# Performance work log

Hardware: AMD Instinct MI355X
Metric: run time of the kernel (lower is better)

Reference implementation:

```python
import jax, jax.numpy as jnp
import numpy as np

N = 50000      # nodes
E = 1600000    # edges (before self loops)
IN = 128
OUT = 128
H = 4
HD = OUT // H  # head dim = 32


def setup_inputs() -> dict:
    key = jax.random.key(0)
    k1, k2, k3, k4, k5 = jax.random.split(key, 5)
    x = jax.random.normal(k1, (N, IN), dtype=jnp.float32)
    edge_index = jax.random.randint(k2, (2, E), 0, N, dtype=jnp.int64)
    # xavier-uniform-ish scales
    W = jax.random.normal(k3, (OUT, IN), dtype=jnp.float32) * (1.0 / np.sqrt(IN))
    att_src = jax.random.normal(k4, (1, H, HD), dtype=jnp.float32) * 0.1
    att_dst = jax.random.normal(k5, (1, H, HD), dtype=jnp.float32) * 0.1
    return {"x": x, "edge_index": edge_index, "W": W, "att_src": att_src, "att_dst": att_dst}


def reference(x, edge_index, W, att_src, att_dst):
    n = x.shape[0]
    # add self loops (tg.utils.add_self_loops appends [i, i] edges)
    loops = jnp.arange(n, dtype=edge_index.dtype)
    ei = jnp.concatenate([edge_index, jnp.stack([loops, loops])], axis=1)
    src, dst = ei[0], ei[1]

    # linear projection, split into heads: [n, H, HD]
    h = (x @ W.T).reshape(n, H, HD)

    # per-node attention logits per head: [n, H]
    a_src = jnp.sum(h * att_src, axis=-1)
    a_dst = jnp.sum(h * att_dst, axis=-1)

    # per-edge attention score: gather + leaky_relu
    alpha = a_src[src] + a_dst[dst]                      # [Etot, H]
    alpha = jax.nn.leaky_relu(alpha, negative_slope=0.2)

    # segment softmax grouped by destination node (numerically stable)
    m = jax.ops.segment_max(alpha, dst, num_segments=n)  # [n, H]
    e = jnp.exp(alpha - m[dst])
    s = jax.ops.segment_sum(e, dst, num_segments=n)      # [n, H]
    e = e / s[dst]                                       # [Etot, H]

    # weighted scatter-add aggregation; f_additive adds 1 to the weights
    msg = h[src] * (e[:, :, None] + 1.0)                 # [Etot, H, HD]
    out = jax.ops.segment_sum(msg, dst, num_segments=n)  # [n, H, HD]
    return out.reshape(n, -1)
```

## Files before the change

### kernel.cpp

```cpp
#include <hip/hip_runtime.h>

#define N_NODES 50000
#define E_EDGES 1600000
#define ETOT    (E_EDGES + N_NODES)
#define DIN  128
#define DOUT 128
#define NH   4
#define HD   32

typedef unsigned short ushort_t;
typedef unsigned int uint_t;
typedef __attribute__((ext_vector_type(8))) short bfrag;
typedef __attribute__((ext_vector_type(4))) float ffrag;

__device__ __forceinline__ ushort_t f2bf(float f) {
  uint_t u = __float_as_uint(f);
  u += 0x7fffu + ((u >> 16) & 1u);
  return (ushort_t)(u >> 16);
}
__device__ __forceinline__ float bf_lo(uint_t u) {
  return __uint_as_float(u << 16);
}
__device__ __forceinline__ float bf_hi(uint_t u) {
  return __uint_as_float(u & 0xffff0000u);
}

#define BSZ   64
#define NBUCK ((N_NODES + BSZ - 1) / BSZ)
#define NBP   1024
#define CAP   2560
#define EPB_A 8192
#define NBLK_A ((ETOT + EPB_A - 1) / EPB_A)
#define NCHUNK 13


__global__ __launch_bounds__(256, 4) void fused_binA_gemm_kernel(
    const int* __restrict__ ei, uint_t* __restrict__ ebuf,
    int* __restrict__ cntm, int* __restrict__ offm,
    const float* __restrict__ x, const float* __restrict__ W,
    const float* __restrict__ att_src, const float* __restrict__ att_dst,
    ushort_t* __restrict__ hb, float* __restrict__ a_src,
    float* __restrict__ a_dst) {
  __shared__ uint_t lds[EPB_A + NBP + 8];
  const int tid = threadIdx.x;

  if (blockIdx.x < NBLK_A) {
    uint_t* stage = lds;
    int* hist = (int*)(lds + EPB_A);
    int* wsum = hist + NBP;
    const int cb = blockIdx.x;
    const int e0 = cb * EPB_A;
    const int n = min(EPB_A, ETOT - e0);
    for (int i = tid; i < NBP; i += 256) hist[i] = 0;
    __syncthreads();
    for (int i = tid; i < n; i += 256) {
      int e = e0 + i;
      int si, di;
      if (e < E_EDGES) { si = ei[e]; di = ei[E_EDGES + e]; }
      else             { si = e - E_EDGES; di = si; }
      stage[i] = ((uint_t)di << 16) | (uint_t)si;
      atomicAdd(&hist[di >> 6], 1);
    }
    __syncthreads();
    const int ln = tid & 63, wv = tid >> 6;
    int c0 = hist[4 * tid], c1 = hist[4 * tid + 1];
    int c2 = hist[4 * tid + 2], c3 = hist[4 * tid + 3];
    int p1 = c0, p2 = c0 + c1, p3 = c0 + c1 + c2;
    int tot = p3 + c3;
    int xx = tot;
#pragma unroll
    for (int off = 1; off < 64; off <<= 1) {
      int y = __shfl_up(xx, off, 64);
      if (ln >= off) xx += y;
    }
    if (ln == 63) wsum[wv] = xx;
    __syncthreads();
    if (tid < 4) {
      int w = wsum[tid];
#pragma unroll
      for (int off = 1; off < 4; off <<= 1) {
        int y = __shfl_up(w, off, 64);
        if (tid >= off) w += y;
      }
      wsum[tid] = w;
    }
    __syncthreads();
    const int wo = (wv == 0) ? 0 : wsum[wv - 1];
    const int base = wo + xx - tot;
#pragma unroll
    for (int k = 0; k < 4; k++) {
      int idx = 4 * tid + k;
      int c = k == 0 ? c0 : k == 1 ? c1 : k == 2 ? c2 : c3;
      int o = base + (k == 0 ? 0 : k == 1 ? p1 : k == 2 ? p2 : p3);
      if (idx < NBUCK) {
        cntm[(size_t)cb * NBP + idx] = c;
        offm[(size_t)cb * NBP + idx] = o;
      }
      hist[idx] = o;
    }
    __syncthreads();
    for (int i = tid; i < n; i += 256) {
      uint_t p = stage[i];
      int pos = atomicAdd(&hist[p >> 22], 1);
      if (pos >= 0 && pos < n) ebuf[e0 + pos] = p;
    }
    return;
  }

  ushort_t* Ws = (ushort_t*)lds;
  const int gb = blockIdx.x - NBLK_A;
  const int wv = tid >> 6, l = tid & 63;
  const int lr = l & 15, lg = l >> 4;
  const int nbase = gb * 64 + wv * 16;
  int na = nbase + lr;
  if (na >= N_NODES) na = N_NODES - 1;
  const float* xrow = x + (size_t)na * DIN;

  float4 px[8];
#pragma unroll
  for (int kt = 0; kt < 4; kt++) {
    px[kt * 2]     = *(const float4*)&xrow[kt * 32 + lg * 8];
    px[kt * 2 + 1] = *(const float4*)&xrow[kt * 32 + lg * 8 + 4];
  }

  for (int u = tid; u < 2048; u += 256) {
    int row = u >> 4;
    float4 w0 = *(const float4*)&W[u * 8];
    float4 w1 = *(const float4*)&W[u * 8 + 4];
    uint4 pk;
    pk.x = (uint_t)f2bf(w0.x) | ((uint_t)f2bf(w0.y) << 16);
    pk.y = (uint_t)f2bf(w0.z) | ((uint_t)f2bf(w0.w) << 16);
    pk.z = (uint_t)f2bf(w1.x) | ((uint_t)f2bf(w1.y) << 16);
    pk.w = (uint_t)f2bf(w1.z) | ((uint_t)f2bf(w1.w) << 16);
    *(uint4*)&Ws[(u ^ (row & 7)) * 8] = pk;
  }
  __syncthreads();

  ffrag acc[8];
#pragma unroll
  for (int oc = 0; oc < 8; oc++) acc[oc] = (ffrag){0.f, 0.f, 0.f, 0.f};

#pragma unroll
  for (int kt = 0; kt < 4; kt++) {
    const float4 x0 = px[kt * 2];
    const float4 x1 = px[kt * 2 + 1];
    bfrag a;
    a[0] = (short)f2bf(x0.x); a[1] = (short)f2bf(x0.y);
    a[2] = (short)f2bf(x0.z); a[3] = (short)f2bf(x0.w);
    a[4] = (short)f2bf(x1.x); a[5] = (short)f2bf(x1.y);
    a[6] = (short)f2bf(x1.z); a[7] = (short)f2bf(x1.w);
#pragma unroll
    for (int oc = 0; oc < 8; oc++) {
      const int u = ((oc * 16 + lr) << 4) + kt * 4 + lg;
      const bfrag b = *(const bfrag*)&Ws[(u ^ (lr & 7)) * 8];
      acc[oc] = __builtin_amdgcn_mfma_f32_16x16x32_bf16(a, b, acc[oc], 0, 0, 0);
    }
  }

#pragma unroll
  for (int oc = 0; oc < 8; oc++) {
#pragma unroll
    for (int j = 0; j < 4; j++) {
      int n = nbase + lg * 4 + j;
      if (n < N_NODES)
        hb[((size_t)n << 7) + oc * 16 + lr] = f2bf(acc[oc][j]);
    }
  }

  float asv[8], adv[8];
#pragma unroll
  for (int oc = 0; oc < 8; oc++) {
    asv[oc] = att_src[oc * 16 + lr];
    adv[oc] = att_dst[oc * 16 + lr];
  }
#pragma unroll
  for (int j = 0; j < 4; j++) {
    float ps[4] = {0.f, 0.f, 0.f, 0.f};
    float pd[4] = {0.f, 0.f, 0.f, 0.f};
#pragma unroll
    for (int oc = 0; oc < 8; oc++) {
      ps[oc >> 1] = fmaf(acc[oc][j], asv[oc], ps[oc >> 1]);
      pd[oc >> 1] = fmaf(acc[oc][j], adv[oc], pd[oc >> 1]);
    }
#pragma unroll
    for (int off = 1; off < 16; off <<= 1) {
#pragma unroll
      for (int hd = 0; hd < 4; hd++) {
        ps[hd] += __shfl_xor(ps[hd], off);
        pd[hd] += __shfl_xor(pd[hd], off);
      }
    }
    int n = nbase + lg * 4 + j;
    if (n < N_NODES && lr < 4) {
      float vs = lr == 0 ? ps[0] : lr == 1 ? ps[1] : lr == 2 ? ps[2] : ps[3];
      float vd = lr == 0 ? pd[0] : lr == 1 ? pd[1] : lr == 2 ? pd[2] : pd[3];
      a_src[n * NH + lr] = vs;
      a_dst[n * NH + lr] = vd;
    }
  }
}

__global__ __launch_bounds__(256) void binB_kernel(
    const uint_t* __restrict__ ebuf, const int* __restrict__ cntm,
    const int* __restrict__ offm,
    int* __restrict__ rs, int* __restrict__ re, ushort_t* __restrict__ col) {
  __shared__ uint_t el[CAP];
  __shared__ int cnt_l[BSZ * NCHUNK];
  __shared__ int roff_l[BSZ * NCHUNK];
  __shared__ int wsum[4];
  const int b = blockIdx.x;
  const int tid = threadIdx.x;
  const int ln = tid & 63, wv = tid >> 6;
  const int n0 = b << 6;
  const int nn = min(BSZ, N_NODES - n0);

  int c = (tid < NBLK_A) ? cntm[(size_t)tid * NBP + b] : 0;
  int o = (tid < NBLK_A) ? offm[(size_t)tid * NBP + b] : 0;
  int xx = c;
#pragma unroll
  for (int off = 1; off < 64; off <<= 1) {
    int y = __shfl_up(xx, off, 64);
    if (ln >= off) xx += y;
  }
  if (ln == 63) wsum[wv] = xx;
  __syncthreads();
  if (tid < 4) {
    int w = wsum[tid];
#pragma unroll
    for (int off = 1; off < 4; off <<= 1) {
      int y = __shfl_up(w, off, 64);
      if (tid >= off) w += y;
    }
    wsum[tid] = w;
  }
  __syncthreads();
  const int wo = (wv == 0) ? 0 : wsum[wv - 1];
  const int mystart = wo + xx - c;
  const int total0 = wsum[3];
  const int total = total0 < CAP ? total0 : CAP;
  if (tid < NBLK_A) {
    const uint_t* src = ebuf + (size_t)tid * EPB_A + o;
    for (int j = 0; j < c; j++) {
      int d = mystart + j;
      if (d < CAP) el[d] = src[j];
    }
  }
  for (int k = tid; k < BSZ * NCHUNK; k += 256) cnt_l[k] = 0;
  __syncthreads();

  for (int i = tid; i < total; i += 256) {
    uint_t p = el[i];
    int key = (int)((p >> 16) & 63) * NCHUNK + (int)((p & 0xFFFFu) >> 12);
    atomicAdd(&cnt_l[key], 1);
  }
  __syncthreads();
  if (tid < BSZ) {
    int pref[NCHUNK];
    int tot = 0;
#pragma unroll
    for (int k = 0; k < NCHUNK; k++) { pref[k] = tot; tot += cnt_l[tid * NCHUNK + k]; }
    int x2 = tot;
#pragma unroll
    for (int off = 1; off < 64; off <<= 1) {
      int y = __shfl_up(x2, off, 64);
      if (tid >= off) x2 += y;
    }
    const int nodebase = x2 - tot;
#pragma unroll
    for (int k = 0; k < NCHUNK; k++) roff_l[tid * NCHUNK + k] = nodebase + pref[k];
    if (tid < nn) {
      rs[n0 + tid] = b * CAP + nodebase;
      re[n0 + tid] = b * CAP + nodebase + tot;
    }
  }
  __syncthreads();
  for (int k = tid; k < BSZ * NCHUNK; k += 256) cnt_l[k] = 0;
  __syncthreads();
  for (int i = tid; i < total; i += 256) {
    uint_t p = el[i];
    int si = (int)(p & 0xFFFFu);
    int key = (int)((p >> 16) & 63) * NCHUNK + (si >> 12);
    int pos = atomicAdd(&cnt_l[key], 1);
    int q = b * CAP + roff_l[key] + pos;
    if (q >= 0 && q < NBUCK * CAP) col[q] = (ushort_t)si;
  }
}

#define NPB 16
#define CH  16

__global__ __launch_bounds__(256, 8) void agg_kernel(
    const ushort_t* __restrict__ col, const int* __restrict__ rs,
    const int* __restrict__ re, const ushort_t* __restrict__ hb,
    const float* __restrict__ a_src, const float* __restrict__ a_dst,
    float* __restrict__ out) {
  __shared__ float w_lds[NPB][CH][NH];
  __shared__ int   si_lds[NPB][CH];
  const int tid  = threadIdx.x;
  const int slot = tid >> 4;
  const int t    = tid & 15;
  const int node = blockIdx.x * NPB + slot;
  const int start = rs[node];
  const int deg   = re[node] - start;
  const float4 ad = *(const float4*)(a_dst + (size_t)node * NH);

  const int head = t >> 2;
  const int c8 = t << 3;
  const ushort_t* hc = hb + c8;
  float s = 0.f;
  float a0 = 0.f, a1 = 0.f, a2 = 0.f, a3 = 0.f;
  float a4 = 0.f, a5 = 0.f, a6 = 0.f, a7 = 0.f;
  float b0 = 0.f, b1 = 0.f, b2 = 0.f, b3 = 0.f;
  float b4 = 0.f, b5 = 0.f, b6 = 0.f, b7 = 0.f;

  int   si_c = 0;
  float4 as_c = make_float4(0.f, 0.f, 0.f, 0.f);
  if (t < deg) {
    si_c = col[start + t];
    si_c = si_c < N_NODES ? si_c : 0;
    as_c = *(const float4*)(a_src + (size_t)si_c * NH);
  }

  for (int base_e = 0; base_e < deg; base_e += CH) {
    int nch = deg - base_e;
    if (nch > CH) nch = CH;
    if (t < nch) {
      si_lds[slot][t] = si_c;
      float v0 = as_c.x + ad.x; v0 = v0 > 0.f ? v0 : 0.2f * v0;
      float v1 = as_c.y + ad.y; v1 = v1 > 0.f ? v1 : 0.2f * v1;
      float v2 = as_c.z + ad.z; v2 = v2 > 0.f ? v2 : 0.2f * v2;
      float v3 = as_c.w + ad.w; v3 = v3 > 0.f ? v3 : 0.2f * v3;
      w_lds[slot][t][0] = __expf(v0);
      w_lds[slot][t][1] = __expf(v1);
      w_lds[slot][t][2] = __expf(v2);
      w_lds[slot][t][3] = __expf(v3);
    }
    __builtin_amdgcn_fence(__ATOMIC_ACQ_REL, "wavefront");
    int nb = base_e + CH;
    if (nb + t < deg) {
      int sn = col[start + nb + t];
      sn = sn < N_NODES ? sn : 0;
      si_c = sn;
      as_c = *(const float4*)(a_src + (size_t)sn * NH);
    }
#pragma unroll 2
    for (int j = 0; j < nch; j++) {
      int si = si_lds[slot][j];
      float e = w_lds[slot][j][head];
      s += e;
      const uint4 hv = *(const uint4*)(hc + ((size_t)si << 7));
      float h0 = bf_lo(hv.x), h1 = bf_hi(hv.x);
      float h2 = bf_lo(hv.y), h3 = bf_hi(hv.y);
      float h4 = bf_lo(hv.z), h5 = bf_hi(hv.z);
      float h6 = bf_lo(hv.w), h7 = bf_hi(hv.w);
      a0 = fmaf(h0, e, a0); b0 += h0;
      a1 = fmaf(h1, e, a1); b1 += h1;
      a2 = fmaf(h2, e, a2); b2 += h2;
      a3 = fmaf(h3, e, a3); b3 += h3;
      a4 = fmaf(h4, e, a4); b4 += h4;
      a5 = fmaf(h5, e, a5); b5 += h5;
      a6 = fmaf(h6, e, a6); b6 += h6;
      a7 = fmaf(h7, e, a7); b7 += h7;
    }
    __builtin_amdgcn_fence(__ATOMIC_ACQ_REL, "wavefront");
  }
  const float inv = 1.0f / s;
  float* op = out + ((size_t)node << 7) + c8;
  *(float4*)(op)     = make_float4(fmaf(a0, inv, b0), fmaf(a1, inv, b1),
                                   fmaf(a2, inv, b2), fmaf(a3, inv, b3));
  *(float4*)(op + 4) = make_float4(fmaf(a4, inv, b4), fmaf(a5, inv, b5),
                                   fmaf(a6, inv, b6), fmaf(a7, inv, b7));
}

extern "C" void kernel_launch(void* const* d_in, const int* in_sizes, int n_in,
                              void* d_out, int out_size, void* d_ws, size_t ws_size,
                              hipStream_t stream) {
  const float* x       = (const float*)d_in[0];
  const int*   ei      = (const int*)d_in[1];
  const float* W       = (const float*)d_in[2];
  const float* att_src = (const float*)d_in[3];
  const float* att_dst = (const float*)d_in[4];
  float* out = (float*)d_out;

  ushort_t* hb = (ushort_t*)d_ws;
  float* a_src = (float*)(hb + (size_t)N_NODES * DOUT);
  float* a_dst = a_src + (size_t)N_NODES * NH;
  int* cntm    = (int*)(a_dst + (size_t)N_NODES * NH);
  int* offm    = cntm + (size_t)NBLK_A * NBP;
  int* rs      = offm + (size_t)NBLK_A * NBP;
  int* re      = rs + N_NODES;
  ushort_t* col = (ushort_t*)(re + N_NODES);
  uint_t* ebuf = (uint_t*)(col + (size_t)NBUCK * CAP);

  const int gemm_blocks = (N_NODES + 63) / 64;
  fused_binA_gemm_kernel<<<NBLK_A + gemm_blocks, 256, 0, stream>>>(
      ei, ebuf, cntm, offm, x, W, att_src, att_dst, hb, a_src, a_dst);
  binB_kernel<<<NBUCK, 256, 0, stream>>>(ebuf, cntm, offm, rs, re, col);
  agg_kernel<<<N_NODES / NPB, 256, 0, stream>>>(col, rs, re, hb, a_src, a_dst, out);
}
```

Before: 100.3 us.

## Shrink LDS in fused bin/GEMM kernel to raise occupancy

Removes the 8192-entry edge staging buffer from the binning blocks: the scatter pass now re-reads the edge indices from global memory instead of LDS. The GEMM path stages W into LDS in two K-halves of 64 columns so it fits in the smaller buffer. With LDS use down from about 37KB to about 16KB per block, the launch bound goes from 4 to 6 blocks per CU. The cost is a second global read of the edge lists and an extra barrier plus W reload in the GEMM.

```diff
diff --git a/kernel.cpp b/kernel.cpp
--- a/kernel.cpp
+++ b/kernel.cpp
@@ -34,19 +34,18 @@
 #define NCHUNK 13
 
 
-__global__ __launch_bounds__(256, 4) void fused_binA_gemm_kernel(
+__global__ __launch_bounds__(256, 6) void fused_binA_gemm_kernel(
     const int* __restrict__ ei, uint_t* __restrict__ ebuf,
     int* __restrict__ cntm, int* __restrict__ offm,
     const float* __restrict__ x, const float* __restrict__ W,
     const float* __restrict__ att_src, const float* __restrict__ att_dst,
     ushort_t* __restrict__ hb, float* __restrict__ a_src,
     float* __restrict__ a_dst) {
-  __shared__ uint_t lds[EPB_A + NBP + 8];
+  __shared__ uint_t lds[4104];
   const int tid = threadIdx.x;
 
   if (blockIdx.x < NBLK_A) {
-    uint_t* stage = lds;
-    int* hist = (int*)(lds + EPB_A);
+    int* hist = (int*)lds;
     int* wsum = hist + NBP;
     const int cb = blockIdx.x;
     const int e0 = cb * EPB_A;
@@ -55,10 +54,7 @@
     __syncthreads();
     for (int i = tid; i < n; i += 256) {
       int e = e0 + i;
-      int si, di;
-      if (e < E_EDGES) { si = ei[e]; di = ei[E_EDGES + e]; }
-      else             { si = e - E_EDGES; di = si; }
-      stage[i] = ((uint_t)di << 16) | (uint_t)si;
+      int di = (e < E_EDGES) ? ei[E_EDGES + e] : (e - E_EDGES);
       atomicAdd(&hist[di >> 6], 1);
     }
     __syncthreads();
@@ -100,9 +96,13 @@
     }
     __syncthreads();
     for (int i = tid; i < n; i += 256) {
-      uint_t p = stage[i];
-      int pos = atomicAdd(&hist[p >> 22], 1);
-      if (pos >= 0 && pos < n) ebuf[e0 + pos] = p;
+      int e = e0 + i;
+      int si, di;
+      if (e < E_EDGES) { si = ei[e]; di = ei[E_EDGES + e]; }
+      else             { si = e - E_EDGES; di = si; }
+      int pos = atomicAdd(&hist[di >> 6], 1);
+      if (pos >= 0 && pos < n)
+        ebuf[e0 + pos] = ((uint_t)di << 16) | (uint_t)si;
     }
     return;
   }
@@ -123,37 +123,43 @@
     px[kt * 2 + 1] = *(const float4*)&xrow[kt * 32 + lg * 8 + 4];
   }
 
-  for (int u = tid; u < 2048; u += 256) {
-    int row = u >> 4;
-    float4 w0 = *(const float4*)&W[u * 8];
-    float4 w1 = *(const float4*)&W[u * 8 + 4];
-    uint4 pk;
-    pk.x = (uint_t)f2bf(w0.x) | ((uint_t)f2bf(w0.y) << 16);
-    pk.y = (uint_t)f2bf(w0.z) | ((uint_t)f2bf(w0.w) << 16);
-    pk.z = (uint_t)f2bf(w1.x) | ((uint_t)f2bf(w1.y) << 16);
-    pk.w = (uint_t)f2bf(w1.z) | ((uint_t)f2bf(w1.w) << 16);
-    *(uint4*)&Ws[(u ^ (row & 7)) * 8] = pk;
-  }
-  __syncthreads();
-
   ffrag acc[8];
 #pragma unroll
   for (int oc = 0; oc < 8; oc++) acc[oc] = (ffrag){0.f, 0.f, 0.f, 0.f};
 
 #pragma unroll
-  for (int kt = 0; kt < 4; kt++) {
-    const float4 x0 = px[kt * 2];
-    const float4 x1 = px[kt * 2 + 1];
-    bfrag a;
-    a[0] = (short)f2bf(x0.x); a[1] = (short)f2bf(x0.y);
-    a[2] = (short)f2bf(x0.z); a[3] = (short)f2bf(x0.w);
-    a[4] = (short)f2bf(x1.x); a[5] = (short)f2bf(x1.y);
-    a[6] = (short)f2bf(x1.z); a[7] = (short)f2bf(x1.w);
-#pragma unroll
-    for (int oc = 0; oc < 8; oc++) {
-      const int u = ((oc * 16 + lr) << 4) + kt * 4 + lg;
-      const bfrag b = *(const bfrag*)&Ws[(u ^ (lr & 7)) * 8];
-      acc[oc] = __builtin_amdgcn_mfma_f32_16x16x32_bf16(a, b, acc[oc], 0, 0, 0);
+  for (int kh = 0; kh < 2; kh++) {
+    if (kh) __syncthreads();
+    for (int g = tid; g < 1024; g += 256) {
+      int o = g >> 3, idx = g & 7;
+      const float* wp = W + (o << 7) + (kh << 6) + idx * 8;
+      float4 w0 = *(const float4*)wp;
+      float4 w1 = *(const float4*)(wp + 4);
+      uint4 pk;
+      pk.x = (uint_t)f2bf(w0.x) | ((uint_t)f2bf(w0.y) << 16);
+      pk.y = (uint_t)f2bf(w0.z) | ((uint_t)f2bf(w0.w) << 16);
+      pk.z = (uint_t)f2bf(w1.x) | ((uint_t)f2bf(w1.y) << 16);
+      pk.w = (uint_t)f2bf(w1.z) | ((uint_t)f2bf(w1.w) << 16);
+      *(uint4*)&Ws[((o << 3) + (idx ^ (o & 7))) * 8] = pk;
+    }
+    __syncthreads();
+#pragma unroll
+    for (int kth = 0; kth < 2; kth++) {
+      const int kt = (kh << 1) | kth;
+      const float4 x0 = px[kt * 2];
+      const float4 x1 = px[kt * 2 + 1];
+      bfrag a;
+      a[0] = (short)f2bf(x0.x); a[1] = (short)f2bf(x0.y);
+      a[2] = (short)f2bf(x0.z); a[3] = (short)f2bf(x0.w);
+      a[4] = (short)f2bf(x1.x); a[5] = (short)f2bf(x1.y);
+      a[6] = (short)f2bf(x1.z); a[7] = (short)f2bf(x1.w);
+#pragma unroll
+      for (int oc = 0; oc < 8; oc++) {
+        const int o = oc * 16 + lr;
+        const int idx = (kth << 2) | lg;
+        const bfrag b = *(const bfrag*)&Ws[((o << 3) + (idx ^ (o & 7))) * 8];
+        acc[oc] = __builtin_amdgcn_mfma_f32_16x16x32_bf16(a, b, acc[oc], 0, 0, 0);
+      }
     }
   }
 
```

Measured after the change: 105.4 us. +5.1%, slower.
